# Kernel tuning notes

Measured on AMD Instinct MI355X. Metric: run time of the kernel, lower is better.

## Reference

```python
import jax, jax.numpy as jnp
import numpy as np

DIM, NH, WS, SS = 192, 6, 8, 4
B, H, W = 4, 192, 192
MID = max(DIM // 16, 4)
N = WS * WS
HD = DIM // NH
SCALE = HD ** -0.5

def _rel_index():
    coords = np.stack(np.meshgrid(np.arange(WS), np.arange(WS), indexing='ij')).reshape(2, -1)
    rel = (coords[:, :, None] - coords[:, None, :]).transpose(1, 2, 0)
    rel[..., 0] += WS - 1
    rel[..., 1] += WS - 1
    rel[..., 0] *= 2 * WS - 1
    return rel.sum(-1)  # (N, N)

REL_IDX = jnp.asarray(_rel_index())

def _shift_mask():
    img = np.zeros((1, H, W, 1), np.float32)
    sl = (slice(0, -WS), slice(-WS, -SS), slice(-SS, None))
    cnt = 0
    for hs in sl:
        for ws_ in sl:
            img[:, hs, ws_, :] = cnt
            cnt += 1
    mw = img.reshape(1, H // WS, WS, W // WS, WS, 1).transpose(0, 1, 3, 2, 4, 5).reshape(-1, N)
    am = mw[:, None, :] - mw[:, :, None]
    return jnp.asarray(np.where(am != 0, -100.0, 0.0).astype(np.float32))  # (nW, N, N)

MASK = _shift_mask()

def _win_part(x):  # (B,H,W,C) -> (B*nW, N, C)
    Bb, Hh, Ww, C = x.shape
    x = x.reshape(Bb, Hh // WS, WS, Ww // WS, WS, C).transpose(0, 1, 3, 2, 4, 5)
    return x.reshape(-1, N, C)

def _win_rev(x, Bb):  # (B*nW, N, C) -> (B,H,W,C)
    x = x.reshape(Bb, H // WS, W // WS, WS, WS, -1).transpose(0, 1, 3, 2, 4, 5)
    return x.reshape(Bb, H, W, -1)

def _ln(x, g, b):
    mu = x.mean(-1, keepdims=True)
    var = ((x - mu) ** 2).mean(-1, keepdims=True)
    return (x - mu) * jax.lax.rsqrt(var + 1e-5) * g + b

def _conv(x, w, b, groups=1):
    y = jax.lax.conv_general_dilated(x, w, (1, 1), 'SAME',
        dimension_numbers=('NCHW', 'OIHW', 'NCHW'), feature_group_count=groups)
    return y + b[None, :, None, None]

def _gelu(x):
    return jax.nn.gelu(x, approximate=False)  # torch default GELU is exact erf


def setup_inputs() -> dict:
    key = jax.random.key(0)
    ks = jax.random.split(key, 12)
    s = 0.02
    return {
        'x': jax.random.normal(ks[0], (B, DIM, H, W), jnp.float32),
        'norm1_g': jnp.ones((DIM,), jnp.float32),
        'norm1_b': jnp.zeros((DIM,), jnp.float32),
        'qkv_w': jax.random.normal(ks[1], (3 * DIM, DIM), jnp.float32) * s,
        'qkv_b': jnp.zeros((3 * DIM,), jnp.float32),
        'rel_table': jax.random.normal(ks[2], ((2 * WS - 1) ** 2, NH), jnp.float32) * s,
        'norm2_g': jnp.ones((DIM,), jnp.float32),
        'norm2_b': jnp.zeros((DIM,), jnp.float32),
        'mlp_w1': jax.random.normal(ks[3], (4 * DIM, DIM), jnp.float32) * s,
        'mlp_b1': jnp.zeros((4 * DIM,), jnp.float32),
        'mlp_w2': jax.random.normal(ks[4], (DIM, 4 * DIM), jnp.float32) * s,
        'mlp_b2': jnp.zeros((DIM,), jnp.float32),
        'ca_c1_w': jax.random.normal(ks[5], (DIM, DIM, 3, 3), jnp.float32) * s,
        'ca_c1_b': jnp.zeros((DIM,), jnp.float32),
        'ca_c2_w': jax.random.normal(ks[6], (DIM, DIM, 3, 3), jnp.float32) * s,
        'ca_c2_b': jnp.zeros((DIM,), jnp.float32),
        'se_w1': jax.random.normal(ks[7], (MID, DIM), jnp.float32) * s,
        'se_b1': jnp.zeros((MID,), jnp.float32),
        'se_w2': jax.random.normal(ks[8], (DIM, MID), jnp.float32) * s,
        'se_b2': jnp.zeros((DIM,), jnp.float32),
        'gate_w': jax.random.normal(ks[9], (DIM, 1, 3, 3), jnp.float32) * s,
        'gate_b': jnp.zeros((DIM,), jnp.float32),
    }


def reference(x, norm1_g, norm1_b, qkv_w, qkv_b, rel_table, norm2_g, norm2_b,
              mlp_w1, mlp_b1, mlp_w2, mlp_b2, ca_c1_w, ca_c1_b, ca_c2_w, ca_c2_b,
              se_w1, se_b1, se_w2, se_b2, gate_w, gate_b):
    Bb = x.shape[0]
    shortcut = x
    xh = _ln(x.transpose(0, 2, 3, 1), norm1_g, norm1_b)  # (B,H,W,C)
    xh = jnp.roll(xh, (-SS, -SS), (1, 2))                # shifted windows
    xw = _win_part(xh)                                   # (B*nW, N, C)
    qkv = jnp.einsum('bnc,dc->bnd', xw, qkv_w) + qkv_b
    qkv = qkv.reshape(-1, N, 3, NH, HD).transpose(2, 0, 3, 1, 4)
    q, k, v = qkv[0], qkv[1], qkv[2]                     # (B_, NH, N, HD)
    attn = jnp.einsum('bhnd,bhmd->bhnm', q * SCALE, k)
    bias = rel_table[REL_IDX.reshape(-1)].reshape(N, N, NH).transpose(2, 0, 1)
    attn = attn + bias[None]
    nW = MASK.shape[0]
    attn = attn.reshape(Bb, nW, NH, N, N) + MASK[None, :, None]
    attn = jax.nn.softmax(attn.reshape(-1, NH, N, N), axis=-1)
    out = jnp.einsum('bhnm,bhmd->bhnd', attn, v).transpose(0, 2, 1, 3).reshape(-1, N, DIM)
    # NOTE: original forward never applies self.proj; faithfully omitted.
    xh = _win_rev(out, Bb)
    xh = jnp.roll(xh, (SS, SS), (1, 2))
    x = shortcut + xh.transpose(0, 3, 1, 2)
    x = x + _conv(x, gate_w, gate_b, groups=DIM)         # depthwise conv gate
    # channel attention (conv body + SE)
    res = x
    y = _conv(x, ca_c1_w, ca_c1_b)
    y = _gelu(y)
    y = _conv(y, ca_c2_w, ca_c2_b)
    p = y.mean((2, 3))                                   # global avg pool -> (B,C)
    wgt = jax.nn.sigmoid(jax.nn.relu(p @ se_w1.T + se_b1) @ se_w2.T + se_b2)
    x = y * wgt[:, :, None, None] + res
    # MLP
    res = x
    xh = _ln(x.transpose(0, 2, 3, 1), norm2_g, norm2_b)
    xh = _gelu(jnp.einsum('bhwc,dc->bhwd', xh, mlp_w1) + mlp_b1)
    xh = jnp.einsum('bhwd,cd->bhwc', xh, mlp_w2) + mlp_b2
    return res + xh.transpose(0, 3, 1, 2)
```

## Files before the change

kernel.cpp:

```cpp
#include <hip/hip_runtime.h>
#include <hip/hip_bf16.h>

#define NWIN 576
#define SP 36864
#define ATT_SCALE 0.17677669529663687f

typedef unsigned short u16;
typedef unsigned int u32;
typedef __attribute__((ext_vector_type(8))) __bf16 bf16x8;
typedef __attribute__((ext_vector_type(4))) float f32x4;

__device__ __forceinline__ float b2f(u16 u){ return __uint_as_float(((u32)u)<<16); }
__device__ __forceinline__ u16 f2b(float f){ u32 u = __float_as_uint(f); return (u16)((u + 0x7FFFu + ((u>>16)&1u)) >> 16); }
__device__ __forceinline__ float fast_rcp(float d){ float r; asm("v_rcp_f32 %0, %1" : "=v"(r) : "v"(d)); return r; }
__device__ __forceinline__ u32 cvtpk(float lo, float hi){ u32 r; asm("v_cvt_pk_bf16_f32 %0, %1, %2" : "=v"(r) : "v"(lo), "v"(hi)); return r; }
__device__ __forceinline__ float gelu_f(float v){
  float u = v*(1.5957691216f + 0.0713548163f*v*v);
  return v * fast_rcp(1.0f + __expf(-u));
}
__device__ __forceinline__ f32x4 mfma16(bf16x8 a, bf16x8 b, f32x4 c){
  return __builtin_amdgcn_mfma_f32_16x16x32_bf16(a, b, c, 0, 0, 0);
}

__global__ __launch_bounds__(256) void k_transpose(const float* __restrict__ x, u16* __restrict__ xn){
  __shared__ float tile[32][33];
  int blk = blockIdx.x;
  int b = blk / 1728; int rem = blk % 1728;
  int hg = rem / 36; int rem2 = rem % 36;
  int wt = rem2 / 6, ct = rem2 % 6;
  int t = threadIdx.x;
  int lw = t & 31, g = t >> 5;
  for (int r4 = 0; r4 < 4; ++r4){
    int h = hg*4 + r4;
    for (int r = 0; r < 4; ++r){
      int cl = g + r*8;
      tile[cl][lw] = x[(((size_t)b*192 + ct*32 + cl)*192 + h)*192 + wt*32 + lw];
    }
    __syncthreads();
    for (int r = 0; r < 4; ++r){
      int wl = g + r*8;
      xn[(((size_t)b*192 + h)*192 + wt*32 + wl)*192 + ct*32 + lw] = f2b(tile[lw][wl]);
    }
    __syncthreads();
  }
}

__global__ __launch_bounds__(256) void k_prep_all(
    const float* __restrict__ c1w, const float* __restrict__ c2w,
    const float* __restrict__ qkv_w, const float* __restrict__ rel_table,
    const float* __restrict__ mlp_w1, const float* __restrict__ mlp_w2,
    const float* __restrict__ n2g, const float* __restrict__ n2b, const float* __restrict__ mb1,
    u16* __restrict__ Wpk1, u16* __restrict__ Wpk2, u16* __restrict__ Qkvpk,
    float* __restrict__ biasT, u16* __restrict__ W1pk, u16* __restrict__ W2pk,
    float* __restrict__ w1gd, float* __restrict__ wcv){
  int i = blockIdx.x*256 + threadIdx.x;
  if (i < 331776){
    int j = i & 7; int l = (i >> 3) & 63; int rem = i >> 9;
    int nt = rem % 12; int rem2 = rem / 12; int kc = rem2 % 6; int tap = rem2 / 6;
    int ci = kc*32 + ((l>>4)<<3) + j;
    int co = nt*16 + (l & 15);
    Wpk1[i] = f2b(c1w[(co*192 + ci)*9 + tap]);
    Wpk2[i] = f2b(c2w[(co*192 + ci)*9 + tap]);
    return;
  }
  i -= 331776;
  if (i < 110592){
    int j = i & 7; int l = (i >> 3) & 63; int rem = i >> 9;
    int kc = rem % 6; int nt = rem / 6;
    int row = nt*16 + (l & 15); int c = kc*32 + ((l>>4)<<3) + j;
    Qkvpk[i] = f2b(qkv_w[row*192 + c]);
    return;
  }
  i -= 110592;
  if (i < 24576){
    int q = i & 63; int k = (i>>6) & 63; int h = i >> 12;
    int di = (q>>3) - (k>>3) + 7; int dj = (q&7) - (k&7) + 7;
    biasT[i] = rel_table[(di*15 + dj)*6 + h];
    return;
  }
  i -= 24576;
  if (i < 147456){
    int j = i & 7; int l = (i >> 3) & 63; int rem = i >> 9;
    int kc = rem % 6; int nt = rem / 6;
    int ho = nt*16 + (l & 15); int ci = kc*32 + ((l>>4)<<3) + j;
    W1pk[i] = f2b(mlp_w1[ho*192 + ci] * n2g[ci]);
    return;
  }
  i -= 147456;
  if (i < 147456){
    int j = i & 7; int l = (i >> 3) & 63; int rem = i >> 9;
    int kc = rem % 24; int nt = rem / 24;
    int co = nt*16 + (l & 15); int ho = kc*32 + ((l>>4)<<3) + j;
    W2pk[i] = f2b(mlp_w2[co*768 + ho]);
    return;
  }
  i -= 147456;
  if (i < 768){
    float sg = 0.f, sb = 0.f;
    const float* row = mlp_w1 + (size_t)i*192;
    for (int ci = 0; ci < 192; ++ci){ float w = row[ci]; sg += w*n2g[ci]; sb += w*n2b[ci]; }
    w1gd[i] = sg; wcv[i] = sb + mb1[i];
  }
}

__global__ __launch_bounds__(768, 3) void k_attn(const float* __restrict__ x, const u16* __restrict__ xn, int use_xn,
    const float* __restrict__ g1, const float* __restrict__ be1,
    const u16* __restrict__ qkvpk, const float* __restrict__ qkv_b,
    const float* __restrict__ biasT, u16* __restrict__ x1)
{
  __shared__ u16 xw[12800];
  __shared__ u16 qs[6][64][40];
  __shared__ u16 ks[6][64][40];
  __shared__ u16 vt[6][32][72];
  __shared__ int ih[64], iw[64], rid[64];
  __shared__ float red[64][12], red2[64][12], mu[64], rsg[64];
  int blk = blockIdx.x, t = threadIdx.x;
  int b = blk / NWIN, wi = blk % NWIN, wy = wi / 24, wx = wi % 24;
  int wid = t >> 6, l = t & 63, l15 = l & 15, lg = l >> 4;
  if (t < 64){
    int i = t >> 3, j = t & 7;
    int gh = wy*8 + i, gw = wx*8 + j;
    int hf = gh + 4; if (hf >= 192) hf -= 192;
    int wf = gw + 4; if (wf >= 192) wf -= 192;
    ih[t] = hf; iw[t] = wf;
    int rh = (gh < 184) ? 0 : ((gh < 188) ? 1 : 2);
    int rw = (gw < 184) ? 0 : ((gw < 188) ? 1 : 2);
    rid[t] = rh*3 + rw;
  }
  __syncthreads();
  if (use_xn){
    for (int idx = t; idx < 1536; idx += 768){
      int n = idx / 24, q = idx % 24;
      *(uint4*)&xw[n*200 + q*8] =
        *(const uint4*)(xn + ((size_t)((b*192 + ih[n])*192 + iw[n]))*192 + q*8);
    }
  } else {
    for (int idx = t; idx < 12288; idx += 768){
      int n = idx & 63, c = idx >> 6;
      xw[n*200 + c] = f2b(x[(((size_t)b*192 + c)*192 + ih[n])*192 + iw[n]]);
    }
  }
  __syncthreads();
  { int n = t / 12, part = t % 12;
    float s = 0.f, s2 = 0.f;
    for (int c = part*16; c < part*16 + 16; ++c){ float v = b2f(xw[n*200 + c]); s += v; s2 += v*v; }
    red[n][part] = s; red2[n][part] = s2; }
  __syncthreads();
  if (t < 64){
    float s = 0.f, s2 = 0.f;
    #pragma unroll
    for (int p = 0; p < 12; ++p){ s += red[t][p]; s2 += red2[t][p]; }
    float m = s * (1.f/192.f);
    float v = s2 * (1.f/192.f) - m*m;
    mu[t] = m; rsg[t] = rsqrtf(v + 1e-5f);
  }
  __syncthreads();
  for (int idx = t; idx < 12288; idx += 768){
    int n = idx & 63, c = idx >> 6;
    float v = (b2f(xw[n*200 + c]) - mu[n]) * rsg[n] * g1[c] + be1[c];
    xw[n*200 + c] = f2b(v);
  }
  __syncthreads();
  {
    f32x4 acc[3][4];
    #pragma unroll
    for (int i3 = 0; i3 < 3; ++i3)
      #pragma unroll
      for (int mt = 0; mt < 4; ++mt) acc[i3][mt] = (f32x4){0.f,0.f,0.f,0.f};
    #pragma unroll
    for (int kc = 0; kc < 6; ++kc){
      bf16x8 a4[4];
      #pragma unroll
      for (int mt = 0; mt < 4; ++mt)
        a4[mt] = *(const bf16x8*)&xw[(mt*16 + l15)*200 + kc*32 + lg*8];
      #pragma unroll
      for (int i3 = 0; i3 < 3; ++i3){
        int ntg = wid*3 + i3;
        bf16x8 bf = *(const bf16x8*)(qkvpk + ((size_t)ntg*6 + kc)*512 + l*8);
        __builtin_amdgcn_s_setprio(1);
        #pragma unroll
        for (int mt = 0; mt < 4; ++mt)
          acc[i3][mt] = mfma16(a4[mt], bf, acc[i3][mt]);
        __builtin_amdgcn_s_setprio(0);
      }
    }
    #pragma unroll
    for (int i3 = 0; i3 < 3; ++i3){
      int ntg = wid*3 + i3;
      float bv = qkv_b[ntg*16 + l15];
      int m = ntg/12, hh = (ntg%12)>>1, hd0 = (ntg&1)*16;
      #pragma unroll
      for (int mt = 0; mt < 4; ++mt)
        #pragma unroll
        for (int r = 0; r < 4; ++r){
          int tok = mt*16 + lg*4 + r;
          float val = acc[i3][mt][r] + bv;
          if (m == 0){ qs[hh][tok][hd0 + l15] = f2b(val * ATT_SCALE); }
          else if (m == 1){ ks[hh][tok][hd0 + l15] = f2b(val); }
          else { vt[hh][hd0 + l15][tok] = f2b(val); }
        }
    }
  }
  __syncthreads();
  int h = wid >> 1, mt0 = (wid & 1) * 2;
  f32x4 st[2][4];
  {
    bf16x8 bq0 = *(const bf16x8*)&qs[h][(mt0  )*16 + l15][lg*8];
    bf16x8 bq1 = *(const bf16x8*)&qs[h][(mt0+1)*16 + l15][lg*8];
    __builtin_amdgcn_s_setprio(1);
    #pragma unroll
    for (int nt = 0; nt < 4; ++nt){
      bf16x8 ak = *(const bf16x8*)&ks[h][nt*16 + l15][lg*8];
      st[0][nt] = mfma16(ak, bq0, (f32x4){0.f,0.f,0.f,0.f});
      st[1][nt] = mfma16(ak, bq1, (f32x4){0.f,0.f,0.f,0.f});
    }
    __builtin_amdgcn_s_setprio(0);
  }
  u32 pk[2][4][2];
  #pragma unroll
  for (int m2 = 0; m2 < 2; ++m2){
    int qg = (mt0 + m2)*16 + l15;
    int rq = rid[qg];
    const float* bp = biasT + (size_t)h*4096 + qg;
    float mx = -1e30f;
    #pragma unroll
    for (int nt = 0; nt < 4; ++nt)
      #pragma unroll
      for (int r = 0; r < 4; ++r){
        int kg = nt*16 + lg*4 + r;
        float v = st[m2][nt][r] + bp[kg*64] + (rq != rid[kg] ? -100.f : 0.f);
        st[m2][nt][r] = v;
        mx = fmaxf(mx, v);
      }
    mx = fmaxf(mx, __shfl_xor(mx, 16));
    mx = fmaxf(mx, __shfl_xor(mx, 32));
    float ssum = 0.f;
    #pragma unroll
    for (int nt = 0; nt < 4; ++nt)
      #pragma unroll
      for (int r = 0; r < 4; ++r){
        float e = __expf(st[m2][nt][r] - mx);
        st[m2][nt][r] = e; ssum += e;
      }
    ssum += __shfl_xor(ssum, 16);
    ssum += __shfl_xor(ssum, 32);
    float inv = fast_rcp(ssum);
    #pragma unroll
    for (int nt = 0; nt < 4; ++nt){
      pk[m2][nt][0] = cvtpk(st[m2][nt][0]*inv, st[m2][nt][1]*inv);
      pk[m2][nt][1] = cvtpk(st[m2][nt][2]*inv, st[m2][nt][3]*inv);
    }
  }
  f32x4 o[2][2];
  #pragma unroll
  for (int m2 = 0; m2 < 2; ++m2)
    #pragma unroll
    for (int nd = 0; nd < 2; ++nd) o[m2][nd] = (f32x4){0.f,0.f,0.f,0.f};
  {
    int srcA = ((lg & 1) << 1)*16 + l15;
    bool hiSel = (lg & 2) != 0;
    #pragma unroll
    for (int kc = 0; kc < 2; ++kc){
      bf16x8 bv0 = *(const bf16x8*)&vt[h][l15][kc*32 + lg*8];
      bf16x8 bv1 = *(const bf16x8*)&vt[h][16 + l15][kc*32 + lg*8];
      #pragma unroll
      for (int m2 = 0; m2 < 2; ++m2){
        u32 q0 = __shfl((int)pk[m2][2*kc  ][0], srcA);
        u32 q1 = __shfl((int)pk[m2][2*kc+1][0], srcA);
        u32 q2 = __shfl((int)pk[m2][2*kc  ][1], srcA);
        u32 q3 = __shfl((int)pk[m2][2*kc+1][1], srcA);
        u32 q4 = __shfl((int)pk[m2][2*kc  ][0], srcA + 16);
        u32 q5 = __shfl((int)pk[m2][2*kc+1][0], srcA + 16);
        u32 q6 = __shfl((int)pk[m2][2*kc  ][1], srcA + 16);
        u32 q7 = __shfl((int)pk[m2][2*kc+1][1], srcA + 16);
        union { u32 u[4]; bf16x8 v; } ap;
        ap.u[0] = hiSel ? q1 : q0;
        ap.u[1] = hiSel ? q3 : q2;
        ap.u[2] = hiSel ? q5 : q4;
        ap.u[3] = hiSel ? q7 : q6;
        __builtin_amdgcn_s_setprio(1);
        o[m2][0] = mfma16(ap.v, bv0, o[m2][0]);
        o[m2][1] = mfma16(ap.v, bv1, o[m2][1]);
        __builtin_amdgcn_s_setprio(0);
      }
    }
  }
  #pragma unroll
  for (int m2 = 0; m2 < 2; ++m2)
    #pragma unroll
    for (int nd = 0; nd < 2; ++nd)
      #pragma unroll
      for (int r = 0; r < 4; ++r){
        int tok = (mt0 + m2)*16 + lg*4 + r;
        xw[tok*200 + h*32 + nd*16 + l15] = f2b(o[m2][nd][r]);
      }
  __syncthreads();
  if (use_xn){
    for (int idx = t; idx < 1536; idx += 768){
      int n = idx / 24, q = idx % 24;
      size_t tokoff = (size_t)((b*192 + ih[n])*192 + iw[n]);
      uint4 xv = *(const uint4*)(xn + tokoff*192 + q*8);
      uint4 ov = *(const uint4*)&xw[n*200 + q*8];
      uint4 res;
      u32* xp = (u32*)&xv; u32* op = (u32*)&ov; u32* rp = (u32*)&res;
      #pragma unroll
      for (int w2 = 0; w2 < 4; ++w2){
        float a0 = b2f((u16)(xp[w2] & 0xffffu)) + b2f((u16)(op[w2] & 0xffffu));
        float a1 = b2f((u16)(xp[w2] >> 16))    + b2f((u16)(op[w2] >> 16));
        rp[w2] = (u32)f2b(a0) | ((u32)f2b(a1) << 16);
      }
      *(uint4*)(x1 + tokoff*192 + q*8) = res;
    }
  } else {
    for (int idx = t; idx < 12288; idx += 768){
      int n = idx & 63, c = idx >> 6;
      size_t tokoff = (size_t)((b*192 + ih[n])*192 + iw[n]);
      float sc = x[(((size_t)b*192 + c)*192 + ih[n])*192 + iw[n]];
      x1[tokoff*192 + c] = f2b(sc + b2f(xw[n*200 + c]));
    }
  }
}

__global__ __launch_bounds__(192) void k_gate(const u16* __restrict__ x1, const float* __restrict__ gw,
                                              const float* __restrict__ gb, u16* __restrict__ x2){
  int bid = blockIdx.x;
  int blk = (bid & 7) * 2304 + (bid >> 3);
  int wt = blk % 24; int rem = blk / 24;
  int h = rem % 192; int b = rem / 192;
  int c = threadIdx.x;
  int w0 = wt*8;
  float wr[9];
  #pragma unroll
  for (int p = 0; p < 9; ++p) wr[p] = gw[c*9 + p];
  float bias = gb[c];
  float in[3][10];
  #pragma unroll
  for (int dy = 0; dy < 3; ++dy){
    int hh = h + dy - 1;
    bool hok = (hh >= 0 && hh < 192);
    #pragma unroll
    for (int p = 0; p < 10; ++p){
      int ww = w0 + p - 1;
      bool ok = hok && (ww >= 0 && ww < 192);
      in[dy][p] = ok ? b2f(x1[(((size_t)b*192 + hh)*192 + ww)*192 + c]) : 0.f;
    }
  }
  size_t rowbase = ((size_t)b*192 + h)*192;
  #pragma unroll
  for (int i = 0; i < 8; ++i){
    float acc = bias;
    #pragma unroll
    for (int dy = 0; dy < 3; ++dy)
      #pragma unroll
      for (int dx = 0; dx < 3; ++dx)
        acc += in[dy][i + dx] * wr[dy*3 + dx];
    float v = in[1][i + 1] + acc;
    x2[(rowbase + w0 + i)*192 + c] = f2b(v);
  }
}

__global__ __launch_bounds__(256) void k_conv(const u16* __restrict__ src, const u16* __restrict__ wpk,
                                              const float* __restrict__ cb, u16* __restrict__ dst,
                                              int do_gelu, float* __restrict__ pp){
  __shared__ u16 tin[20592];
  int bid = blockIdx.x;
  int blk = (bid & 7) * 288 + (bid >> 3);
  int b = blk / 576; int rem = blk % 576;
  int h = rem / 3; int w0 = (rem % 3) * 64;
  int t = threadIdx.x;
  int wid = t >> 6, l = t & 63;
  int l15 = l & 15, lg = l >> 4;
  f32x4 acc[4][3];
  #pragma unroll
  for (int mt = 0; mt < 4; ++mt)
    #pragma unroll
    for (int j = 0; j < 3; ++j) acc[mt][j] = (f32x4){0.f,0.f,0.f,0.f};
  for (int ch = 0; ch < 2; ++ch){
    __syncthreads();
    for (int idx = t; idx < 2376; idx += 256){
      int r = idx / 792; int r2 = idx % 792; int p = r2 / 12; int q = r2 % 12;
      int hh = h + r - 1, ww = w0 + p - 1;
      uint4 v = make_uint4(0u,0u,0u,0u);
      if (hh >= 0 && hh < 192 && ww >= 0 && ww < 192)
        v = *(const uint4*)(src + (((size_t)(b*192 + hh))*192 + ww)*192 + ch*96 + q*8);
      *(uint4*)&tin[(r*66 + p)*104 + q*8] = v;
    }
    __syncthreads();
    for (int dy = 0; dy < 3; ++dy){
      for (int kch = 0; kch < 3; ++kch){
        bf16x8 af[4][3];
        #pragma unroll
        for (int mt = 0; mt < 4; ++mt)
          #pragma unroll
          for (int dx = 0; dx < 3; ++dx)
            af[mt][dx] = *(const bf16x8*)&tin[(dy*66 + mt*16 + l15 + dx)*104 + kch*32 + lg*8];
        bf16x8 bw[3][3];
        int kc = ch*3 + kch;
        #pragma unroll
        for (int dx = 0; dx < 3; ++dx)
          #pragma unroll
          for (int j = 0; j < 3; ++j)
            bw[dx][j] = *(const bf16x8*)(wpk + ((((size_t)(dy*3+dx)*6 + kc)*12 + wid*3 + j)*64 + l)*8);
        __builtin_amdgcn_s_setprio(1);
        #pragma unroll
        for (int dx = 0; dx < 3; ++dx)
          #pragma unroll
          for (int j = 0; j < 3; ++j)
            #pragma unroll
            for (int mt = 0; mt < 4; ++mt)
              acc[mt][j] = mfma16(af[mt][dx], bw[dx][j], acc[mt][j]);
        __builtin_amdgcn_s_setprio(0);
      }
    }
  }
  __syncthreads();
  float bv[3];
  #pragma unroll
  for (int j = 0; j < 3; ++j) bv[j] = cb[wid*48 + j*16 + l15];
  #pragma unroll
  for (int mt = 0; mt < 4; ++mt)
    #pragma unroll
    for (int j = 0; j < 3; ++j)
      #pragma unroll
      for (int r = 0; r < 4; ++r){
        int pix = mt*16 + lg*4 + r;
        float v = acc[mt][j][r] + bv[j];
        if (do_gelu) v = gelu_f(v);
        tin[pix*200 + wid*48 + j*16 + l15] = f2b(v);
      }
  __syncthreads();
  for (int idx = t; idx < 1536; idx += 256){
    int pix = idx / 24, q = idx % 24;
    *(uint4*)(dst + (((size_t)(b*192 + h))*192 + w0 + pix)*192 + q*8) = *(const uint4*)&tin[pix*200 + q*8];
  }
  if (pp){
    if (t < 192){
      float s = 0.f;
      #pragma unroll 8
      for (int pix = 0; pix < 64; ++pix) s += b2f(tin[pix*200 + t]);
      pp[(size_t)blk*192 + t] = s;
    }
  }
}

__global__ __launch_bounds__(256) void k_se(const float* __restrict__ pp, const float* __restrict__ w1,
    const float* __restrict__ bb1, const float* __restrict__ w2, const float* __restrict__ bb2,
    float* __restrict__ wgt){
  __shared__ float pb[192]; __shared__ float hq[12];
  int t = threadIdx.x;
  int b = blockIdx.x;
  if (t < 192){
    float s = 0.f;
    const float* base = pp + (size_t)b*576*192 + t;
    for (int ch = 0; ch < 576; ++ch) s += base[ch*192];
    pb[t] = s * (1.f/36864.f);
  }
  __syncthreads();
  if (t < 12){ float a = bb1[t]; for (int c = 0; c < 192; ++c) a += pb[c]*w1[t*192 + c]; hq[t] = fmaxf(a, 0.f); }
  __syncthreads();
  if (t < 192){ float a = bb2[t]; for (int m = 0; m < 12; ++m) a += hq[m]*w2[t*12 + m]; wgt[b*192 + t] = 1.f/(1.f + __expf(-a)); }
}

__global__ __launch_bounds__(256) void k_combine(const u16* __restrict__ y2, const u16* __restrict__ x2,
                                                 const float* __restrict__ wgt, u16* __restrict__ x3){
  size_t e = ((size_t)blockIdx.x*256 + threadIdx.x)*4;
  int c = (int)(e % 192);
  int b = (int)(e / ((size_t)SP*192));
  uint2 ya = *(const uint2*)(y2 + e);
  uint2 xa = *(const uint2*)(x2 + e);
  float4 wf = *(const float4*)(wgt + b*192 + c);
  float r0 = b2f((u16)(ya.x & 0xffffu))*wf.x + b2f((u16)(xa.x & 0xffffu));
  float r1 = b2f((u16)(ya.x >> 16))   *wf.y + b2f((u16)(xa.x >> 16));
  float r2 = b2f((u16)(ya.y & 0xffffu))*wf.z + b2f((u16)(xa.y & 0xffffu));
  float r3 = b2f((u16)(ya.y >> 16))   *wf.w + b2f((u16)(xa.y >> 16));
  uint2 o; o.x = (u32)f2b(r0) | ((u32)f2b(r1)<<16); o.y = (u32)f2b(r2) | ((u32)f2b(r3)<<16);
  *(uint2*)(x3 + e) = o;
}

__global__ __launch_bounds__(256, 2) void k_mlp(const u16* __restrict__ src0, const u16* __restrict__ src1,
    const float* __restrict__ wgt, int fused, const u16* __restrict__ W1pk,
    const float* __restrict__ w1gd, const float* __restrict__ wcv,
    const u16* __restrict__ W2pk, const float* __restrict__ mb2,
    float* __restrict__ out){
  __shared__ u16 lnS[32][200];
  __shared__ u16 hidH[32*384];
  __shared__ float mu[32], rsg[32];
  int blk = blockIdx.x, t = threadIdx.x;
  int b = blk / 1152; int rem = blk % 1152;
  int h = rem / 6; int w0 = (rem % 6) * 32;
  size_t tokbase = ((size_t)b*192 + h)*192 + w0;
  int wid = t >> 6, l = t & 63, l15 = l & 15, lg = l >> 4;
  char* hb = (char*)hidH;
  if (fused){
    for (int idx = t; idx < 768; idx += 256){
      int tok = idx / 24, q = idx % 24;
      uint4 yv = *(const uint4*)(src0 + (tokbase + tok)*192 + q*8);
      uint4 xv = *(const uint4*)(src1 + (tokbase + tok)*192 + q*8);
      const float* wb = wgt + b*192 + q*8;
      uint4 res;
      u32* yp = (u32*)&yv; u32* xp = (u32*)&xv; u32* rp = (u32*)&res;
      #pragma unroll
      for (int w2 = 0; w2 < 4; ++w2){
        float r0 = b2f((u16)(yp[w2] & 0xffffu))*wb[2*w2]   + b2f((u16)(xp[w2] & 0xffffu));
        float r1 = b2f((u16)(yp[w2] >> 16))   *wb[2*w2+1] + b2f((u16)(xp[w2] >> 16));
        rp[w2] = cvtpk(r0, r1);
      }
      *(uint4*)&lnS[tok][q*8] = res;
    }
  } else {
    for (int idx = t; idx < 768; idx += 256){
      int tok = idx / 24, q = idx % 24;
      *(uint4*)&lnS[tok][q*8] = *(const uint4*)(src0 + (tokbase + tok)*192 + q*8);
    }
  }
  __syncthreads();
  { int tok = t >> 3, part = t & 7;
    float s = 0.f, s2 = 0.f;
    #pragma unroll
    for (int i = 0; i < 3; ++i){
      uint4 v = *(const uint4*)&lnS[tok][part*8 + 64*i];
      u32* vp = (u32*)&v;
      #pragma unroll
      for (int q = 0; q < 4; ++q){
        float a = b2f((u16)(vp[q] & 0xffffu)), c2 = b2f((u16)(vp[q] >> 16));
        s += a + c2; s2 += a*a + c2*c2;
      }
    }
    #pragma unroll
    for (int d = 1; d < 8; d <<= 1){
      s  += __shfl_xor(s, d);
      s2 += __shfl_xor(s2, d);
    }
    if (part == 0){
      float m = s*(1.f/192.f); float v = s2*(1.f/192.f) - m*m;
      mu[tok] = m; rsg[tok] = rsqrtf(v + 1e-5f);
    } }
  __syncthreads();
  float rsgL[2], rmuL[2];
  rsgL[0] = rsg[l15];      rmuL[0] = rsgL[0]*mu[l15];
  rsgL[1] = rsg[16 + l15]; rmuL[1] = rsgL[1]*mu[16 + l15];
  bf16x8 bT[2][6];
  #pragma unroll
  for (int tt = 0; tt < 2; ++tt)
    #pragma unroll
    for (int kc = 0; kc < 6; ++kc)
      bT[tt][kc] = *(const bf16x8*)&lnS[tt*16 + l15][kc*32 + lg*8];
  int nb = wid*3;
  f32x4 acc2[2][3];
  #pragma unroll
  for (int mt = 0; mt < 2; ++mt)
    #pragma unroll
    for (int j = 0; j < 3; ++j) acc2[mt][j] = (f32x4){0.f,0.f,0.f,0.f};
  #pragma unroll
  for (int ph = 0; ph < 2; ++ph){
    #pragma unroll
    for (int i = 0; i < 6; ++i){
      int hot = ph*24 + wid*6 + i;
      bf16x8 aw[6];
      #pragma unroll
      for (int kc = 0; kc < 6; ++kc)
        aw[kc] = *(const bf16x8*)(W1pk + ((size_t)(hot*6 + kc)*64 + l)*8);
      float4 gd = *(const float4*)(w1gd + hot*16 + lg*4);
      float4 wc4 = *(const float4*)(wcv + hot*16 + lg*4);
      int hoL = (wid*6 + i)*16 + lg*4;
      #pragma unroll
      for (int tt = 0; tt < 2; ++tt){
        f32x4 acc = (f32x4){0.f,0.f,0.f,0.f};
        __builtin_amdgcn_s_setprio(1);
        #pragma unroll
        for (int kc = 0; kc < 6; ++kc)
          acc = mfma16(aw[kc], bT[tt][kc], acc);
        __builtin_amdgcn_s_setprio(0);
        float h0 = fmaf(rsgL[tt], acc[0], fmaf(-rmuL[tt], gd.x, wc4.x));
        float h1 = fmaf(rsgL[tt], acc[1], fmaf(-rmuL[tt], gd.y, wc4.y));
        float h2 = fmaf(rsgL[tt], acc[2], fmaf(-rmuL[tt], gd.z, wc4.z));
        float h3 = fmaf(rsgL[tt], acc[3], fmaf(-rmuL[tt], gd.w, wc4.w));
        u32 p0 = cvtpk(gelu_f(h0), gelu_f(h1));
        u32 p1 = cvtpk(gelu_f(h2), gelu_f(h3));
        int tok = tt*16 + l15;
        int byt = (tok*768 + hoL*2) ^ ((l15 & 7) << 4);
        *(uint2*)(hb + byt) = make_uint2(p0, p1);
      }
    }
    __syncthreads();
    #pragma unroll 2
    for (int kc = 0; kc < 12; ++kc){
      int by0 = ((      l15)*768 + (kc*32 + lg*8)*2) ^ ((l15 & 7) << 4);
      int by1 = ((16 +  l15)*768 + (kc*32 + lg*8)*2) ^ ((l15 & 7) << 4);
      bf16x8 a0 = *(const bf16x8*)(hb + by0);
      bf16x8 a1 = *(const bf16x8*)(hb + by1);
      bf16x8 bw3[3];
      #pragma unroll
      for (int j = 0; j < 3; ++j)
        bw3[j] = *(const bf16x8*)(W2pk + (((size_t)(nb + j)*24 + ph*12 + kc)*64 + l)*8);
      __builtin_amdgcn_s_setprio(1);
      #pragma unroll
      for (int j = 0; j < 3; ++j){
        acc2[0][j] = mfma16(a0, bw3[j], acc2[0][j]);
        acc2[1][j] = mfma16(a1, bw3[j], acc2[1][j]);
      }
      __builtin_amdgcn_s_setprio(0);
    }
    __syncthreads();
  }
  #pragma unroll
  for (int j = 0; j < 3; ++j){
    int co = (nb + j)*16 + l15;
    float bj = mb2[co];
    #pragma unroll
    for (int mt = 0; mt < 2; ++mt){
      int tok0 = mt*16 + lg*4;
      float4 ov;
      #pragma unroll
      for (int r = 0; r < 4; ++r)
        ((float*)&ov)[r] = b2f(lnS[tok0 + r][co]) + acc2[mt][j][r] + bj;
      *(float4*)(out + (((size_t)b*192 + co)*192 + h)*192 + w0 + tok0) = ov;
    }
  }
}

extern "C" void kernel_launch(void* const* d_in, const int* in_sizes, int n_in,
                              void* d_out, int out_size, void* d_ws, size_t ws_size,
                              hipStream_t stream){
  const float* x      = (const float*)d_in[0];
  const float* n1g    = (const float*)d_in[1];
  const float* n1b    = (const float*)d_in[2];
  const float* qkv_w  = (const float*)d_in[3];
  const float* qkv_b  = (const float*)d_in[4];
  const float* rel_t  = (const float*)d_in[5];
  const float* n2g    = (const float*)d_in[6];
  const float* n2b    = (const float*)d_in[7];
  const float* mlp_w1 = (const float*)d_in[8];
  const float* mlp_b1 = (const float*)d_in[9];
  const float* mlp_w2 = (const float*)d_in[10];
  const float* mlp_b2 = (const float*)d_in[11];
  const float* c1w    = (const float*)d_in[12];
  const float* c1b    = (const float*)d_in[13];
  const float* c2w    = (const float*)d_in[14];
  const float* c2b    = (const float*)d_in[15];
  const float* sew1   = (const float*)d_in[16];
  const float* seb1   = (const float*)d_in[17];
  const float* sew2   = (const float*)d_in[18];
  const float* seb2   = (const float*)d_in[19];
  const float* gw     = (const float*)d_in[20];
  const float* gb     = (const float*)d_in[21];

  const size_t E  = (size_t)4*192*192*192;
  const size_t EB = E*2;
  const size_t SMALL = 663552*2 + 221184 + 98304 + 294912*2 + 4*576*192*4 + 768*4*3 + 65536;
  char* ws = (char*)d_ws;
  u16* ws0 = (u16*)(ws);
  u16* ws1 = (u16*)(ws + EB);
  size_t off = 2*EB;
  int use_xn = (ws_size >= 3*EB + SMALL) ? 1 : 0;
  u16* xn = nullptr;
  if (use_xn){ xn = (u16*)(ws + off); off += EB; }
  u16* Wpk1  = (u16*)(ws + off); off += 663552;
  u16* Wpk2  = (u16*)(ws + off); off += 663552;
  u16* Qkvpk = (u16*)(ws + off); off += 221184;
  float* biasT = (float*)(ws + off); off += 98304;
  u16* W1pk = (u16*)(ws + off); off += 294912;
  u16* W2pk = (u16*)(ws + off); off += 294912;
  float* w1gd = (float*)(ws + off); off += 768*4;
  float* wcv  = (float*)(ws + off); off += 768*4;
  float* pp  = (float*)(ws + off); off += (size_t)4*576*192*4;
  float* wgt = (float*)(ws + off); off += 768*4;

  if (use_xn) k_transpose<<<6912, 256, 0, stream>>>(x, xn);
  k_prep_all<<<2979, 256, 0, stream>>>(c1w, c2w, qkv_w, rel_t, mlp_w1, mlp_w2,
                                       n2g, n2b, mlp_b1,
                                       Wpk1, Wpk2, Qkvpk, biasT, W1pk, W2pk, w1gd, wcv);

  k_attn<<<2304, 768, 0, stream>>>(x, xn, use_xn, n1g, n1b, Qkvpk, qkv_b, biasT, ws0);
  k_gate<<<18432, 192, 0, stream>>>(ws0, gw, gb, ws1);
  k_conv<<<2304, 256, 0, stream>>>(ws1, Wpk1, c1b, ws0, 1, nullptr);
  u16* y2 = use_xn ? xn : (u16*)d_out;
  k_conv<<<2304, 256, 0, stream>>>(ws0, Wpk2, c2b, y2, 0, pp);
  k_se<<<4, 256, 0, stream>>>(pp, sew1, seb1, sew2, seb2, wgt);
  if (use_xn){
    k_mlp<<<4608, 256, 0, stream>>>(y2, ws1, wgt, 1, W1pk, w1gd, wcv, W2pk, mlp_b2, (float*)d_out);
  } else {
    k_combine<<<27648, 256, 0, stream>>>((const u16*)d_out, ws1, wgt, ws0);
    k_mlp<<<4608, 256, 0, stream>>>(ws0, ws0, wgt, 0, W1pk, w1gd, wcv, W2pk, mlp_b2, (float*)d_out);
  }
}
```

Measured before the change: 589.7 us.

## Process two output rows per conv block to reuse weights and halo

The 3x3 conv kernel now computes two output rows of 64 pixels per block instead of one. It loads a 4-row halo tile and reuses each weight fragment across 8 M-tiles, which halves weight loads per output and shares the halo rows between the two outputs. The grid and the SE partial-sum count are halved to match. Separately, the setprio hints around the MFMAs in the attention kernel are removed. In exchange, accumulator registers double and LDS use grows, which may lower occupancy.

```diff
diff --git a/kernel.cpp b/kernel.cpp
--- a/kernel.cpp
+++ b/kernel.cpp
@@ -177,11 +177,9 @@
       for (int i3 = 0; i3 < 3; ++i3){
         int ntg = wid*3 + i3;
         bf16x8 bf = *(const bf16x8*)(qkvpk + ((size_t)ntg*6 + kc)*512 + l*8);
-        __builtin_amdgcn_s_setprio(1);
         #pragma unroll
         for (int mt = 0; mt < 4; ++mt)
           acc[i3][mt] = mfma16(a4[mt], bf, acc[i3][mt]);
-        __builtin_amdgcn_s_setprio(0);
       }
     }
     #pragma unroll
@@ -207,14 +205,12 @@
   {
     bf16x8 bq0 = *(const bf16x8*)&qs[h][(mt0  )*16 + l15][lg*8];
     bf16x8 bq1 = *(const bf16x8*)&qs[h][(mt0+1)*16 + l15][lg*8];
-    __builtin_amdgcn_s_setprio(1);
     #pragma unroll
     for (int nt = 0; nt < 4; ++nt){
       bf16x8 ak = *(const bf16x8*)&ks[h][nt*16 + l15][lg*8];
       st[0][nt] = mfma16(ak, bq0, (f32x4){0.f,0.f,0.f,0.f});
       st[1][nt] = mfma16(ak, bq1, (f32x4){0.f,0.f,0.f,0.f});
     }
-    __builtin_amdgcn_s_setprio(0);
   }
   u32 pk[2][4][2];
   #pragma unroll
@@ -278,10 +274,8 @@
         ap.u[1] = hiSel ? q3 : q2;
         ap.u[2] = hiSel ? q5 : q4;
         ap.u[3] = hiSel ? q7 : q6;
-        __builtin_amdgcn_s_setprio(1);
         o[m2][0] = mfma16(ap.v, bv0, o[m2][0]);
         o[m2][1] = mfma16(ap.v, bv1, o[m2][1]);
-        __builtin_amdgcn_s_setprio(0);
       }
     }
   }
@@ -362,24 +356,25 @@
 __global__ __launch_bounds__(256) void k_conv(const u16* __restrict__ src, const u16* __restrict__ wpk,
                                               const float* __restrict__ cb, u16* __restrict__ dst,
                                               int do_gelu, float* __restrict__ pp){
-  __shared__ u16 tin[20592];
+  __shared__ u16 tin[27456];
   int bid = blockIdx.x;
-  int blk = (bid & 7) * 288 + (bid >> 3);
-  int b = blk / 576; int rem = blk % 576;
-  int h = rem / 3; int w0 = (rem % 3) * 64;
+  int blk = (bid & 7) * 144 + (bid >> 3);
+  int b = blk / 288; int rem = blk % 288;
+  int hp = rem / 3; int w0 = (rem % 3) * 64;
+  int h0 = hp*2;
   int t = threadIdx.x;
   int wid = t >> 6, l = t & 63;
   int l15 = l & 15, lg = l >> 4;
-  f32x4 acc[4][3];
-  #pragma unroll
-  for (int mt = 0; mt < 4; ++mt)
+  f32x4 acc[8][3];
+  #pragma unroll
+  for (int mt = 0; mt < 8; ++mt)
     #pragma unroll
     for (int j = 0; j < 3; ++j) acc[mt][j] = (f32x4){0.f,0.f,0.f,0.f};
   for (int ch = 0; ch < 2; ++ch){
     __syncthreads();
-    for (int idx = t; idx < 2376; idx += 256){
+    for (int idx = t; idx < 3168; idx += 256){
       int r = idx / 792; int r2 = idx % 792; int p = r2 / 12; int q = r2 % 12;
-      int hh = h + r - 1, ww = w0 + p - 1;
+      int hh = h0 + r - 1, ww = w0 + p - 1;
       uint4 v = make_uint4(0u,0u,0u,0u);
       if (hh >= 0 && hh < 192 && ww >= 0 && ww < 192)
         v = *(const uint4*)(src + (((size_t)(b*192 + hh))*192 + ww)*192 + ch*96 + q*8);
@@ -388,28 +383,28 @@
     __syncthreads();
     for (int dy = 0; dy < 3; ++dy){
       for (int kch = 0; kch < 3; ++kch){
-        bf16x8 af[4][3];
-        #pragma unroll
-        for (int mt = 0; mt < 4; ++mt)
-          #pragma unroll
-          for (int dx = 0; dx < 3; ++dx)
-            af[mt][dx] = *(const bf16x8*)&tin[(dy*66 + mt*16 + l15 + dx)*104 + kch*32 + lg*8];
-        bf16x8 bw[3][3];
         int kc = ch*3 + kch;
         #pragma unroll
-        for (int dx = 0; dx < 3; ++dx)
+        for (int dx = 0; dx < 3; ++dx){
+          bf16x8 bw[3];
           #pragma unroll
           for (int j = 0; j < 3; ++j)
-            bw[dx][j] = *(const bf16x8*)(wpk + ((((size_t)(dy*3+dx)*6 + kc)*12 + wid*3 + j)*64 + l)*8);
-        __builtin_amdgcn_s_setprio(1);
-        #pragma unroll
-        for (int dx = 0; dx < 3; ++dx)
+            bw[j] = *(const bf16x8*)(wpk + ((((size_t)(dy*3+dx)*6 + kc)*12 + wid*3 + j)*64 + l)*8);
+          bf16x8 af[8];
+          #pragma unroll
+          for (int mt = 0; mt < 8; ++mt){
+            int row = (mt >> 2) + dy;
+            int p = (mt & 3)*16 + l15 + dx;
+            af[mt] = *(const bf16x8*)&tin[(row*66 + p)*104 + kch*32 + lg*8];
+          }
+          __builtin_amdgcn_s_setprio(1);
           #pragma unroll
           for (int j = 0; j < 3; ++j)
             #pragma unroll
-            for (int mt = 0; mt < 4; ++mt)
-              acc[mt][j] = mfma16(af[mt][dx], bw[dx][j], acc[mt][j]);
-        __builtin_amdgcn_s_setprio(0);
+            for (int mt = 0; mt < 8; ++mt)
+              acc[mt][j] = mfma16(af[mt], bw[j], acc[mt][j]);
+          __builtin_amdgcn_s_setprio(0);
+        }
       }
     }
   }
@@ -418,26 +413,27 @@
   #pragma unroll
   for (int j = 0; j < 3; ++j) bv[j] = cb[wid*48 + j*16 + l15];
   #pragma unroll
-  for (int mt = 0; mt < 4; ++mt)
+  for (int mt = 0; mt < 8; ++mt)
     #pragma unroll
     for (int j = 0; j < 3; ++j)
       #pragma unroll
       for (int r = 0; r < 4; ++r){
-        int pix = mt*16 + lg*4 + r;
+        int px = mt*16 + lg*4 + r;
         float v = acc[mt][j][r] + bv[j];
         if (do_gelu) v = gelu_f(v);
-        tin[pix*200 + wid*48 + j*16 + l15] = f2b(v);
-      }
-  __syncthreads();
-  for (int idx = t; idx < 1536; idx += 256){
-    int pix = idx / 24, q = idx % 24;
-    *(uint4*)(dst + (((size_t)(b*192 + h))*192 + w0 + pix)*192 + q*8) = *(const uint4*)&tin[pix*200 + q*8];
+        tin[px*200 + wid*48 + j*16 + l15] = f2b(v);
+      }
+  __syncthreads();
+  for (int idx = t; idx < 3072; idx += 256){
+    int px = idx / 24, q = idx % 24;
+    *(uint4*)(dst + (((size_t)(b*192 + h0 + (px>>6)))*192 + w0 + (px & 63))*192 + q*8) =
+      *(const uint4*)&tin[px*200 + q*8];
   }
   if (pp){
     if (t < 192){
       float s = 0.f;
       #pragma unroll 8
-      for (int pix = 0; pix < 64; ++pix) s += b2f(tin[pix*200 + t]);
+      for (int px = 0; px < 128; ++px) s += b2f(tin[px*200 + t]);
       pp[(size_t)blk*192 + t] = s;
     }
   }
@@ -451,8 +447,8 @@
   int b = blockIdx.x;
   if (t < 192){
     float s = 0.f;
-    const float* base = pp + (size_t)b*576*192 + t;
-    for (int ch = 0; ch < 576; ++ch) s += base[ch*192];
+    const float* base = pp + (size_t)b*288*192 + t;
+    for (int ch = 0; ch < 288; ++ch) s += base[ch*192];
     pb[t] = s * (1.f/36864.f);
   }
   __syncthreads();
@@ -673,9 +669,9 @@
 
   k_attn<<<2304, 768, 0, stream>>>(x, xn, use_xn, n1g, n1b, Qkvpk, qkv_b, biasT, ws0);
   k_gate<<<18432, 192, 0, stream>>>(ws0, gw, gb, ws1);
-  k_conv<<<2304, 256, 0, stream>>>(ws1, Wpk1, c1b, ws0, 1, nullptr);
+  k_conv<<<1152, 256, 0, stream>>>(ws1, Wpk1, c1b, ws0, 1, nullptr);
   u16* y2 = use_xn ? xn : (u16*)d_out;
-  k_conv<<<2304, 256, 0, stream>>>(ws0, Wpk2, c2b, y2, 0, pp);
+  k_conv<<<1152, 256, 0, stream>>>(ws0, Wpk2, c2b, y2, 0, pp);
   k_se<<<4, 256, 0, stream>>>(pp, sew1, seb1, sew2, seb2, wgt);
   if (use_xn){
     k_mlp<<<4608, 256, 0, stream>>>(y2, ws1, wgt, 1, W1pk, w1gd, wcv, W2pk, mlp_b2, (float*)d_out);
```

Measured after the change: 618.8 us. +4.9%, slower.
